# Optimization experiments

Hardware: AMD Instinct MI355X
Metric: run time of the kernel (lower is better)

## Reference

```python
import jax, jax.numpy as jnp
import numpy as np

N_NODES = 100000
N_EDGES = 3200000
D = 128
K = 10
NITER = 10


def kmeans(x, K=K, Niter=NITER):
    # c init = first K points, Lloyd iterations (matches the LazyTensor KMeans math)
    N, Dm = x.shape
    c = x[:K, :]
    cl = jnp.zeros((N,), dtype=jnp.int32)
    for _ in range(Niter):
        # argmin_j ||x_i - c_j||^2 == argmin_j (-2 x_i.c_j + ||c_j||^2)
        d = -2.0 * (x @ c.T) + jnp.sum(c * c, axis=-1)  # [N, K]
        cl = jnp.argmin(d, axis=1)
        counts = jax.ops.segment_sum(jnp.ones((N,), x.dtype), cl, num_segments=K)
        sums = jax.ops.segment_sum(x, cl, num_segments=K)
        c = sums / jnp.maximum(counts, 1.0)[:, None]  # guard empty clusters
    return cl, c


def scatter_softmax(scores, seg_ids, num_segments):
    # numerically-stable softmax over edges grouped by seg_ids (torch_geometric.utils.softmax)
    seg_max = jax.ops.segment_max(scores, seg_ids, num_segments=num_segments)
    shifted = jnp.exp(scores - seg_max[seg_ids])
    seg_sum = jax.ops.segment_sum(shifted, seg_ids, num_segments=num_segments)
    return shifted / (seg_sum[seg_ids] + 1e-16)


def setup_inputs() -> dict:
    key = jax.random.key(0)
    k1, k2, k3, k4, k5 = jax.random.split(key, 5)
    x = jax.random.normal(k1, (N_NODES, D), dtype=jnp.float32)
    edge = jax.random.randint(k2, (2, N_EDGES), 0, N_NODES, dtype=jnp.int64)
    # xavier_normal gain 1.414 on [D, D]: std = gain * sqrt(2 / (fan_in + fan_out))
    std = 1.414 * np.sqrt(2.0 / (D + D))
    WQ = jax.random.normal(k3, (D, D), dtype=jnp.float32) * std
    WV = jax.random.normal(k4, (D, D), dtype=jnp.float32) * std
    WK = jax.random.normal(k5, (D, D), dtype=jnp.float32) * std
    return {"x": x, "edge": edge, "WQ": WQ, "WV": WV, "WK": WK}


def reference(x, edge, WQ, WV, WK):
    attention_norm_idx = 0
    alloc, centroids = kmeans(x)                      # [N], [K, D]
    q = centroids @ WQ                                 # [K, D]
    v = centroids @ WV                                 # [K, D]
    prods = (q @ v.T) / jnp.sqrt(jnp.asarray(WK.shape[1], x.dtype))  # [K, K]
    centroid_attention = jax.nn.softmax(prods, axis=1)
    src_c = alloc[edge[0, :]]                          # [E]
    dst_c = alloc[edge[1, :]]                          # [E]
    edge_attention = centroid_attention[src_c, dst_c]  # [E] gather
    attention = scatter_softmax(edge_attention, edge[attention_norm_idx], N_NODES)
    return attention
```

## Files before the change

### kernel.cpp

```cpp
#include <hip/hip_runtime.h>

#define NN 100000
#define NE 3200000
#define DD 128
#define KC 10
#define NITER 10
#define NBK 1024
#define NPAIR (NN / 2)
#define NB4 (NPAIR / 4)
#define NE4 (NE / 4)
#define NWX 512

template <int CTRL, int RM>
__device__ __forceinline__ float dppadd(float v) {
  int t = __builtin_amdgcn_update_dpp(0, __builtin_bit_cast(int, v), CTRL, RM,
                                      0xF, true);
  return v + __builtin_bit_cast(float, t);
}

__device__ __forceinline__ float halfsum_tail(float v) {
  v = dppadd<0x111, 0xF>(v);
  v = dppadd<0x112, 0xF>(v);
  v = dppadd<0x114, 0xF>(v);
  v = dppadd<0x118, 0xF>(v);
  v = dppadd<0x142, 0xA>(v);
  return v;
}
__device__ __forceinline__ int bcast31i(int v) {
  return __builtin_amdgcn_ds_swizzle(v, 0x3E0);
}

__global__ __launch_bounds__(256, 2) void k_iter6(
    const float* __restrict__ x, const float* __restrict__ csrc,
    float* __restrict__ partial, float* __restrict__ cntpart,
    unsigned char* __restrict__ cl8, int last) {
  __shared__ float cs[KC][DD];
  __shared__ float wsum[4][KC][DD];
  __shared__ float wcnt[4][KC];
  const int tid = threadIdx.x;
  float* wsf = (float*)wsum;
  for (int i = tid; i < KC * DD; i += 256) ((float*)cs)[i] = csrc[i];
  for (int i = tid; i < 4 * KC * DD; i += 256) wsf[i] = 0.f;
  __syncthreads();
  const int w = tid >> 6, lane = tid & 63, half = lane >> 5, hl = lane & 31;

  float4 cfrag[KC];
  float bias[KC];
#pragma unroll
  for (int j = 0; j < KC; ++j) {
    const float4 c4 = *(const float4*)&cs[j][hl * 4];
    cfrag[j] = c4;
    bias[j] = -0.5f * (c4.x * c4.x + c4.y * c4.y + c4.z * c4.z + c4.w * c4.w);
  }
  unsigned int cntlo = 0, cnthi = 0;

  float* const wrow = &wsum[w][0][hl * 4];
  const float4* __restrict__ x4 = (const float4*)x;

  const int xcd = blockIdx.x & 7;
  const int wk = (blockIdx.x >> 3) * 4 + w;
  const int bs = (xcd * NB4) / 8;
  const int be = ((xcd + 1) * NB4) / 8;

  float4 vA[4], vB[4];

  auto compute = [&](const float4* v, int B) {
#pragma unroll
    for (int u = 0; u < 4; ++u) {
      const int row = 8 * B + 2 * u + half;
      float d[KC];
#pragma unroll
      for (int j = 0; j < KC; ++j)
        d[j] = bias[j] + v[u].x * cfrag[j].x + v[u].y * cfrag[j].y +
               v[u].z * cfrag[j].z + v[u].w * cfrag[j].w;
#pragma unroll
      for (int j = 0; j < KC; ++j) d[j] = halfsum_tail(d[j]);
      int best = 0;
      float bd = d[0];
#pragma unroll
      for (int j = 1; j < KC; ++j) {
        if (d[j] > bd) { bd = d[j]; best = j; }
      }
      const int bown = bcast31i(best);
      const int bother = __shfl_xor(bown, 32);
      const unsigned sh = 6u * (unsigned)bown;
      cntlo += (bown < 5) ? (1u << sh) : 0u;
      cnthi += (bown >= 5) ? (1u << (sh - 30u)) : 0u;
      if (last && hl == 0) cl8[row] = (unsigned char)bown;

      if (bown == bother) {
        float4 vs;
        vs.x = v[u].x + __shfl_xor(v[u].x, 32);
        vs.y = v[u].y + __shfl_xor(v[u].y, 32);
        vs.z = v[u].z + __shfl_xor(v[u].z, 32);
        vs.w = v[u].w + __shfl_xor(v[u].w, 32);
        if (half == 0) {
          float4 t = *(float4*)&wrow[bown * DD];
          t.x += vs.x; t.y += vs.y; t.z += vs.z; t.w += vs.w;
          *(float4*)&wrow[bown * DD] = t;
        }
      } else {
        float4 t = *(float4*)&wrow[bown * DD];
        t.x += v[u].x; t.y += v[u].y; t.z += v[u].z; t.w += v[u].w;
        *(float4*)&wrow[bown * DD] = t;
      }
    }
  };
  auto loadb = [&](float4* v, int B) {
    const size_t rb = (size_t)(8 * B) * 32;
#pragma unroll
    for (int u = 0; u < 4; ++u) v[u] = x4[rb + (size_t)(2 * u + half) * 32 + hl];
  };

  int B = bs + wk;
  if (B < be) {
    loadb(vA, B);
    for (;;) {
      if (B + NWX < be) loadb(vB, B + NWX);
      compute(vA, B);
      B += NWX;
      if (B >= be) break;
      if (B + NWX < be) loadb(vA, B + NWX);
      compute(vB, B);
      B += NWX;
      if (B >= be) break;
    }
  }
  __syncthreads();
  for (int i = tid; i < KC * DD; i += 256)
    partial[(size_t)blockIdx.x * (KC * DD) + i] =
        wsf[i] + wsf[KC * DD + i] + wsf[2 * KC * DD + i] + wsf[3 * KC * DD + i];
  cntlo += __shfl_xor(cntlo, 32);
  cnthi += __shfl_xor(cnthi, 32);
  if (lane == 0) {
#pragma unroll
    for (int j = 0; j < 5; ++j) {
      wcnt[w][j] = (float)((cntlo >> (6 * j)) & 63u);
      wcnt[w][j + 5] = (float)((cnthi >> (6 * j)) & 63u);
    }
  }
  __syncthreads();
  if (tid < KC)
    cntpart[blockIdx.x * KC + tid] =
        wcnt[0][tid] + wcnt[1][tid] + wcnt[2][tid] + wcnt[3][tid];
}

__global__ __launch_bounds__(256) void k_update2(
    const float* __restrict__ partial, const float* __restrict__ cntpart,
    float* __restrict__ c) {
  const int j = blockIdx.x >> 4, q = blockIdx.x & 15;
  const int tid = threadIdx.x;
  __shared__ float creds[256];
  __shared__ float red2[32][8];
  float cf = 0.f;
#pragma unroll
  for (int m = 0; m < NBK / 256; ++m) cf += cntpart[(tid + 256 * m) * KC + j];
  creds[tid] = cf;
  __syncthreads();
  for (int s = 128; s > 0; s >>= 1) {
    if (tid < s) creds[tid] += creds[tid + s];
    __syncthreads();
  }
  const float denom = fmaxf(creds[0], 1.f);
  const int cc = tid & 7, r = tid >> 3;
  const int col = j * DD + q * 8 + cc;
  float s0 = 0.f;
#pragma unroll 8
  for (int m = 0; m < NBK / 32; ++m)
    s0 += partial[(size_t)(r + 32 * m) * (KC * DD) + col];
  red2[r][cc] = s0;
  __syncthreads();
  if (tid < 8) {
    float t = 0.f;
#pragma unroll
    for (int rr = 0; rr < 32; ++rr) t += red2[rr][tid];
    c[j * DD + q * 8 + tid] = t / denom;
  }
}

__global__ __launch_bounds__(DD) void k_qv(const float* __restrict__ c,
                                           const float* __restrict__ WQ,
                                           const float* __restrict__ WV,
                                           float* __restrict__ qv) {
  const int b = blockIdx.x;
  const int mat = b / KC, i = b % KC;
  const float* __restrict__ W = mat ? WV : WQ;
  __shared__ float cr[DD];
  const int k = threadIdx.x;
  cr[k] = c[i * DD + k];
  __syncthreads();
  float a = 0.f;
#pragma unroll 8
  for (int m = 0; m < DD; ++m) a += cr[m] * W[m * DD + k];
  qv[(size_t)mat * KC * DD + i * DD + k] = a;
}

__global__ __launch_bounds__(DD) void k_att(const float* __restrict__ qv,
                                            float* __restrict__ CA) {
  __shared__ float q[KC][DD + 2], v[KC][DD + 2], pr[KC][KC];
  const int tid = threadIdx.x;
  for (int i = 0; i < KC; ++i) {
    q[i][tid] = qv[i * DD + tid];
    v[i][tid] = qv[KC * DD + i * DD + tid];
  }
  __syncthreads();
  if (tid < KC * KC) {
    const int i = tid / KC, l = tid % KC;
    float acc = 0.f;
#pragma unroll 8
    for (int m = 0; m < DD; ++m) acc += q[i][m] * v[l][m];
    pr[i][l] = acc / sqrtf((float)DD);
  }
  __syncthreads();
  if (tid < KC) {
    float mx = pr[tid][0];
    for (int l = 1; l < KC; ++l) mx = fmaxf(mx, pr[tid][l]);
    float e[KC];
    float s = 0.f;
    for (int l = 0; l < KC; ++l) {
      e[l] = expf(pr[tid][l] - mx);
      s += e[l];
    }
    for (int l = 0; l < KC; ++l) CA[tid * KC + l] = e[l] / s;
  }
}

__global__ __launch_bounds__(256) void k_cnt(const int* __restrict__ e0,
                                             const int* __restrict__ e1,
                                             const unsigned char* __restrict__ cl8,
                                             int* __restrict__ cnt, int base) {
  const int i = base + blockIdx.x * 256 + threadIdx.x;
  if (i >= NE4) return;
  const int4 a = ((const int4*)e0)[i];
  const int4 b = ((const int4*)e1)[i];
  atomicAdd(&cnt[(size_t)a.x * KC + cl8[b.x]], 1);
  atomicAdd(&cnt[(size_t)a.y * KC + cl8[b.y]], 1);
  atomicAdd(&cnt[(size_t)a.z * KC + cl8[b.z]], 1);
  atomicAdd(&cnt[(size_t)a.w * KC + cl8[b.w]], 1);
}

__global__ __launch_bounds__(256) void k_tab2(
    const unsigned char* __restrict__ cl8, const int* __restrict__ cnt,
    const float* __restrict__ CA, float2* __restrict__ den2) {
  __shared__ float cas[KC * KC];
  __shared__ float rm[KC];
  if (threadIdx.x < KC * KC) cas[threadIdx.x] = CA[threadIdx.x];
  __syncthreads();
  if (threadIdx.x < KC) {
    float m = cas[threadIdx.x * KC];
    for (int l = 1; l < KC; ++l) m = fmaxf(m, cas[threadIdx.x * KC + l]);
    rm[threadIdx.x] = m;
  }
  __syncthreads();
  const int n = blockIdx.x * 256 + threadIdx.x;
  if (n >= NN) return;
  const int s = cl8[n];
  const float m = rm[s];
  float dsum = 0.f;
#pragma unroll
  for (int j = 0; j < KC; ++j) {
    const int cj = cnt[(size_t)n * KC + j];
    dsum += (float)cj * expf(cas[s * KC + j] - m);
  }
  den2[n] = float2{dsum, (float)s};
}

__global__ __launch_bounds__(256) void k_gather2(
    const int* __restrict__ e0, const int* __restrict__ e1,
    const unsigned char* __restrict__ cl8, const float* __restrict__ CA,
    const float2* __restrict__ den2, float* __restrict__ out) {
  __shared__ float cas[KC * KC];
  __shared__ float rm[KC];
  if (threadIdx.x < KC * KC) cas[threadIdx.x] = CA[threadIdx.x];
  __syncthreads();
  if (threadIdx.x < KC) {
    float m = cas[threadIdx.x * KC];
    for (int l = 1; l < KC; ++l) m = fmaxf(m, cas[threadIdx.x * KC + l]);
    rm[threadIdx.x] = m;
  }
  __syncthreads();
  const int i = blockIdx.x * 256 + threadIdx.x;
  const int4 a = ((const int4*)e0)[i];
  const int4 b = ((const int4*)e1)[i];
  float4 r;
  {
    const float2 dc = den2[a.x];
    const int s = (int)dc.y;
    r.x = expf(cas[s * KC + cl8[b.x]] - rm[s]) / (dc.x + 1e-16f);
  }
  {
    const float2 dc = den2[a.y];
    const int s = (int)dc.y;
    r.y = expf(cas[s * KC + cl8[b.y]] - rm[s]) / (dc.x + 1e-16f);
  }
  {
    const float2 dc = den2[a.z];
    const int s = (int)dc.y;
    r.z = expf(cas[s * KC + cl8[b.z]] - rm[s]) / (dc.x + 1e-16f);
  }
  {
    const float2 dc = den2[a.w];
    const int s = (int)dc.y;
    r.w = expf(cas[s * KC + cl8[b.w]] - rm[s]) / (dc.x + 1e-16f);
  }
  ((float4*)out)[i] = r;
}

extern "C" void kernel_launch(void* const* d_in, const int* in_sizes, int n_in,
                              void* d_out, int out_size, void* d_ws,
                              size_t ws_size, hipStream_t stream) {
  const float* x = (const float*)d_in[0];
  const int* edge = (const int*)d_in[1];
  const float* WQ = (const float*)d_in[2];
  const float* WV = (const float*)d_in[3];
  float* out = (float*)d_out;
  const int* e0 = edge;
  const int* e1 = edge + NE;

  float* ws = (float*)d_ws;
  float* c = ws;
  float* CA = ws + 1280;
  float* qv = ws + 1392;
  float2* den2 = (float2*)(qv + 2 * KC * DD);
  float* partial = (float*)(den2 + NN);
  float* cntpart = partial + (size_t)NBK * KC * DD;
  int* cnt = (int*)(cntpart + NBK * KC);
  unsigned char* cl8 = (unsigned char*)(cnt + (size_t)NN * KC);

  hipMemsetAsync(cnt, 0, (size_t)NN * KC * sizeof(int), stream);

  for (int it = 0; it < NITER; ++it) {
    const float* csrc = (it == 0) ? x : c;
    k_iter6<<<NBK, 256, 0, stream>>>(x, csrc, partial, cntpart, cl8,
                                     it == NITER - 1);
    k_update2<<<KC * 16, 256, 0, stream>>>(partial, cntpart, c);
  }
  k_qv<<<2 * KC, DD, 0, stream>>>(c, WQ, WV, qv);
  k_att<<<1, DD, 0, stream>>>(qv, CA);
  const int TOT_BLKS = (NE4 + 255) / 256;
  const int QB8 = (TOT_BLKS + 7) / 8;
  for (int q = 0; q < 8; ++q) {
    const int nb = (q < 7) ? QB8 : (TOT_BLKS - 7 * QB8);
    k_cnt<<<nb, 256, 0, stream>>>(e0, e1, cl8, cnt, q * QB8 * 256);
  }
  k_tab2<<<(NN + 255) / 256, 256, 0, stream>>>(cl8, cnt, CA, den2);
  k_gather2<<<NE4 / 256, 256, 0, stream>>>(e0, e1, cl8, CA, den2, out);
}
```

Measured before the change: 496.0 us.

## Split centroid partial reduction into two stages and widen gather per thread

Adds an intermediate reduction kernel that folds the 1024 per-block centroid partials into 128, so the update kernel reads far fewer rows per column with more parallelism across the grid. The tab kernel loads per-node counts as int2 pairs, and the gather kernel handles two int4 edge groups per thread so more independent random loads are in flight. The cost is an extra kernel launch per k-means iteration and more registers per thread in the gather.

```diff
diff --git a/kernel.cpp b/kernel.cpp
--- a/kernel.cpp
+++ b/kernel.cpp
@@ -10,6 +10,7 @@
 #define NB4 (NPAIR / 4)
 #define NE4 (NE / 4)
 #define NWX 512
+#define NR2 128
 
 template <int CTRL, int RM>
 __device__ __forceinline__ float dppadd(float v) {
@@ -145,8 +146,20 @@
         wcnt[0][tid] + wcnt[1][tid] + wcnt[2][tid] + wcnt[3][tid];
 }
 
+__global__ __launch_bounds__(256) void k_red1(const float* __restrict__ partial,
+                                              float* __restrict__ p2) {
+  const int b = blockIdx.x;
+  const size_t base = (size_t)b * 8 * (KC * DD);
+  for (int i = threadIdx.x; i < KC * DD; i += 256) {
+    float s = 0.f;
+#pragma unroll
+    for (int m = 0; m < 8; ++m) s += partial[base + (size_t)m * (KC * DD) + i];
+    p2[(size_t)b * (KC * DD) + i] = s;
+  }
+}
+
 __global__ __launch_bounds__(256) void k_update2(
-    const float* __restrict__ partial, const float* __restrict__ cntpart,
+    const float* __restrict__ p2, const float* __restrict__ cntpart,
     float* __restrict__ c) {
   const int j = blockIdx.x >> 4, q = blockIdx.x & 15;
   const int tid = threadIdx.x;
@@ -165,9 +178,9 @@
   const int cc = tid & 7, r = tid >> 3;
   const int col = j * DD + q * 8 + cc;
   float s0 = 0.f;
-#pragma unroll 8
-  for (int m = 0; m < NBK / 32; ++m)
-    s0 += partial[(size_t)(r + 32 * m) * (KC * DD) + col];
+#pragma unroll
+  for (int m = 0; m < NR2 / 32; ++m)
+    s0 += p2[(size_t)(r + 32 * m) * (KC * DD) + col];
   red2[r][cc] = s0;
   __syncthreads();
   if (tid < 8) {
@@ -256,11 +269,13 @@
   if (n >= NN) return;
   const int s = cl8[n];
   const float m = rm[s];
+  const int2* __restrict__ cr = (const int2*)(cnt + (size_t)n * KC);
   float dsum = 0.f;
 #pragma unroll
-  for (int j = 0; j < KC; ++j) {
-    const int cj = cnt[(size_t)n * KC + j];
-    dsum += (float)cj * expf(cas[s * KC + j] - m);
+  for (int h = 0; h < 5; ++h) {
+    const int2 cj = cr[h];
+    dsum += (float)cj.x * expf(cas[s * KC + 2 * h] - m);
+    dsum += (float)cj.y * expf(cas[s * KC + 2 * h + 1] - m);
   }
   den2[n] = float2{dsum, (float)s};
 }
@@ -279,31 +294,59 @@
     rm[threadIdx.x] = m;
   }
   __syncthreads();
-  const int i = blockIdx.x * 256 + threadIdx.x;
-  const int4 a = ((const int4*)e0)[i];
-  const int4 b = ((const int4*)e1)[i];
-  float4 r;
+  const int t = blockIdx.x * 256 + threadIdx.x;
+  const int i0 = t * 2;
+  if (i0 >= NE4) return;
+  const int4 a0 = ((const int4*)e0)[i0];
+  const int4 b0 = ((const int4*)e1)[i0];
+  const bool two = (i0 + 1 < NE4);
+  int4 a1 = a0, b1 = b0;
+  if (two) {
+    a1 = ((const int4*)e0)[i0 + 1];
+    b1 = ((const int4*)e1)[i0 + 1];
+  }
+  const float2 d0 = den2[a0.x], d1 = den2[a0.y], d2 = den2[a0.z],
+               d3 = den2[a0.w], d4 = den2[a1.x], d5 = den2[a1.y],
+               d6 = den2[a1.z], d7 = den2[a1.w];
+  const int c0 = cl8[b0.x], c1 = cl8[b0.y], c2 = cl8[b0.z], c3 = cl8[b0.w],
+            c4 = cl8[b1.x], c5 = cl8[b1.y], c6 = cl8[b1.z], c7 = cl8[b1.w];
+  float4 r0, r1;
   {
-    const float2 dc = den2[a.x];
-    const int s = (int)dc.y;
-    r.x = expf(cas[s * KC + cl8[b.x]] - rm[s]) / (dc.x + 1e-16f);
+    const int s = (int)d0.y;
+    r0.x = expf(cas[s * KC + c0] - rm[s]) / (d0.x + 1e-16f);
   }
   {
-    const float2 dc = den2[a.y];
-    const int s = (int)dc.y;
-    r.y = expf(cas[s * KC + cl8[b.y]] - rm[s]) / (dc.x + 1e-16f);
+    const int s = (int)d1.y;
+    r0.y = expf(cas[s * KC + c1] - rm[s]) / (d1.x + 1e-16f);
   }
   {
-    const float2 dc = den2[a.z];
-    const int s = (int)dc.y;
-    r.z = expf(cas[s * KC + cl8[b.z]] - rm[s]) / (dc.x + 1e-16f);
+    const int s = (int)d2.y;
+    r0.z = expf(cas[s * KC + c2] - rm[s]) / (d2.x + 1e-16f);
   }
   {
-    const float2 dc = den2[a.w];
-    const int s = (int)dc.y;
-    r.w = expf(cas[s * KC + cl8[b.w]] - rm[s]) / (dc.x + 1e-16f);
-  }
-  ((float4*)out)[i] = r;
+    const int s = (int)d3.y;
+    r0.w = expf(cas[s * KC + c3] - rm[s]) / (d3.x + 1e-16f);
+  }
+  ((float4*)out)[i0] = r0;
+  if (two) {
+    {
+      const int s = (int)d4.y;
+      r1.x = expf(cas[s * KC + c4] - rm[s]) / (d4.x + 1e-16f);
+    }
+    {
+      const int s = (int)d5.y;
+      r1.y = expf(cas[s * KC + c5] - rm[s]) / (d5.x + 1e-16f);
+    }
+    {
+      const int s = (int)d6.y;
+      r1.z = expf(cas[s * KC + c6] - rm[s]) / (d6.x + 1e-16f);
+    }
+    {
+      const int s = (int)d7.y;
+      r1.w = expf(cas[s * KC + c7] - rm[s]) / (d7.x + 1e-16f);
+    }
+    ((float4*)out)[i0 + 1] = r1;
+  }
 }
 
 extern "C" void kernel_launch(void* const* d_in, const int* in_sizes, int n_in,
@@ -323,7 +366,8 @@
   float* qv = ws + 1392;
   float2* den2 = (float2*)(qv + 2 * KC * DD);
   float* partial = (float*)(den2 + NN);
-  float* cntpart = partial + (size_t)NBK * KC * DD;
+  float* p2 = partial + (size_t)NBK * KC * DD;
+  float* cntpart = p2 + (size_t)NR2 * KC * DD;
   int* cnt = (int*)(cntpart + NBK * KC);
   unsigned char* cl8 = (unsigned char*)(cnt + (size_t)NN * KC);
 
@@ -333,7 +377,8 @@
     const float* csrc = (it == 0) ? x : c;
     k_iter6<<<NBK, 256, 0, stream>>>(x, csrc, partial, cntpart, cl8,
                                      it == NITER - 1);
-    k_update2<<<KC * 16, 256, 0, stream>>>(partial, cntpart, c);
+    k_red1<<<NR2, 256, 0, stream>>>(partial, p2);
+    k_update2<<<KC * 16, 256, 0, stream>>>(p2, cntpart, c);
   }
   k_qv<<<2 * KC, DD, 0, stream>>>(c, WQ, WV, qv);
   k_att<<<1, DD, 0, stream>>>(qv, CA);
@@ -344,5 +389,6 @@
     k_cnt<<<nb, 256, 0, stream>>>(e0, e1, cl8, cnt, q * QB8 * 256);
   }
   k_tab2<<<(NN + 255) / 256, 256, 0, stream>>>(cl8, cnt, CA, den2);
-  k_gather2<<<NE4 / 256, 256, 0, stream>>>(e0, e1, cl8, CA, den2, out);
-}
+  const int GB = (NE4 / 2 + 255) / 256;
+  k_gather2<<<GB, 256, 0, stream>>>(e0, e1, cl8, CA, den2, out);
+}
```

After: 511.9 us. +3.2%, slower.
